# Optimization experiments

Hardware: AMD Instinct MI355X
Metric: run time of the kernel (lower is better)

The kernel has to match this reference:

```python
import jax, jax.numpy as jnp
import numpy as np

NUM_HEADS = 8
HEAD_SIZE = 64  # hidden_dim // num_heads = 512 // 8
SCALE = 1.0 / np.sqrt(HEAD_SIZE).astype(np.float32)
CAUSAL = True


def setup_inputs() -> dict:
    key = jax.random.key(0)
    k1, k2, k3 = jax.random.split(key, 3)
    b, s, d = 4, 2048, 512
    x = jax.random.normal(k1, (b, s, d), dtype=jnp.float32)
    w_qkv = jax.random.normal(k2, (d, 3 * d), dtype=jnp.float32) * 0.02
    b_qkv = jnp.zeros((3 * d,), dtype=jnp.float32)
    w_out = jax.random.normal(k3, (d, d), dtype=jnp.float32) * 0.02
    b_out = jnp.zeros((d,), dtype=jnp.float32)
    return {"x": x, "w_qkv": w_qkv, "b_qkv": b_qkv, "w_out": w_out, "b_out": b_out}


def reference(x, w_qkv, b_qkv, w_out, b_out):
    b, s, d = x.shape
    h, hd = NUM_HEADS, HEAD_SIZE
    qkv = x @ w_qkv + b_qkv                      # (b, s, 3d)
    q, k, v = jnp.split(qkv, 3, axis=-1)
    # (b, s, d) -> (b, h, s, hd)
    q = q.reshape(b, s, h, hd).transpose(0, 2, 1, 3)
    k = k.reshape(b, s, h, hd).transpose(0, 2, 1, 3)
    v = v.reshape(b, s, h, hd).transpose(0, 2, 1, 3)
    scores = jnp.einsum('bhqd,bhkd->bhqk', q, k) * SCALE  # (b, h, s, s)
    if CAUSAL:
        causal_mask = jnp.triu(jnp.ones((s, s), dtype=bool), k=1)
        scores = jnp.where(causal_mask, -jnp.inf, scores)
    attn = jax.nn.softmax(scores, axis=-1)
    out = jnp.einsum('bhqk,bhkd->bhqd', attn, v)          # (b, h, s, hd)
    out = out.transpose(0, 2, 1, 3).reshape(b, s, d)
    return out @ w_out + b_out
```

## Files before the change

### kernel.cpp

```cpp
#include <hip/hip_runtime.h>
#include <hip/hip_bf16.h>

#define BATCH 4
#define SEQ   2048
#define DM    512
#define NH    8
#define HD    64
#define PART  (BATCH*NH*SEQ*HD)
#define QSCALE 0.18033688f

typedef unsigned short u16;
typedef unsigned int   u32;
typedef __bf16 bf16x8 __attribute__((ext_vector_type(8)));
typedef float  f32x4  __attribute__((ext_vector_type(4)));
typedef float  f32x16 __attribute__((ext_vector_type(16)));
typedef unsigned int u32x2 __attribute__((ext_vector_type(2)));

__device__ __forceinline__ u16 f2bf(float f) {
    union { float f; u32 u; } v; v.f = f;
    u32 r = v.u + 0x7fffu + ((v.u >> 16) & 1u);
    return (u16)(r >> 16);
}

__device__ __forceinline__ void glds16(const u16* g, u16* lds) {
    __builtin_amdgcn_global_load_lds(
        (const __attribute__((address_space(1))) void*)g,
        (__attribute__((address_space(3))) void*)lds, 16, 0, 0);
}

__device__ __forceinline__ void pl32swap(u32 &a, u32 &b) {
    u32x2 r = __builtin_amdgcn_permlane32_swap(a, b, false, false);
    a = r[0]; b = r[1];
}

__global__ __launch_bounds__(256) void prep_k(
    const float* __restrict__ x, u16* __restrict__ xb,
    const float* __restrict__ w_qkv, u16* __restrict__ t_qkv,
    const float* __restrict__ w_out, u16* __restrict__ t_out)
{
    __shared__ u16 Ts[64][72];
    const int z = blockIdx.z, bx = blockIdx.x, t = threadIdx.x;

    if (z == 0) {
        const int n8 = PART / 8;
        for (int i = bx * 256 + t; i < n8; i += 512 * 256) {
            float4 a = *(const float4*)(x + (size_t)i * 8);
            float4 b = *(const float4*)(x + (size_t)i * 8 + 4);
            union { uint4 v; u16 s[8]; } o;
            o.s[0] = f2bf(a.x); o.s[1] = f2bf(a.y);
            o.s[2] = f2bf(a.z); o.s[3] = f2bf(a.w);
            o.s[4] = f2bf(b.x); o.s[5] = f2bf(b.y);
            o.s[6] = f2bf(b.z); o.s[7] = f2bf(b.w);
            *(uint4*)(xb + (size_t)i * 8) = o.v;
        }
        return;
    }
    const int N = (z == 1) ? 3 * DM : DM;
    const int ntiles = N / 64;
    if (bx >= ntiles * 8) return;
    const float* W = (z == 1) ? w_qkv : w_out;
    u16* Wt = (z == 1) ? t_qkv : t_out;
    const int n0 = (bx % ntiles) * 64, k0 = (bx / ntiles) * 64;

    #pragma unroll
    for (int l = 0; l < 4; ++l) {
        int idx = l * 1024 + t * 4;
        int r = idx >> 6, c = idx & 63;
        float4 v = *(const float4*)(W + (size_t)(k0 + r) * N + n0 + c);
        Ts[c + 0][r] = f2bf(v.x);
        Ts[c + 1][r] = f2bf(v.y);
        Ts[c + 2][r] = f2bf(v.z);
        Ts[c + 3][r] = f2bf(v.w);
    }
    __syncthreads();
    #pragma unroll
    for (int l = 0; l < 2; ++l) {
        int idx = l * 256 + t;
        int row = idx >> 3, ch = idx & 7;
        *(uint4*)(Wt + (size_t)(n0 + row) * DM + k0 + ch * 8) =
            *(const uint4*)(&Ts[row][ch * 8]);
    }
}

template<int MODE>
__global__ __launch_bounds__(256) void gemm_k(
    const u16* __restrict__ A, const u16* __restrict__ Bt,
    const float* __restrict__ bias, void* __restrict__ outv,
    int M, int N, int K)
{
    constexpr int BM = (MODE == 1) ? 64 : 128;
    constexpr int NI = (MODE == 1) ? 2 : 4;

    __shared__ __align__(16) u16 As[2][BM * 32];
    __shared__ __align__(16) u16 Bs[2][128 * 32];

    const int tid  = threadIdx.x;
    const int bm0  = blockIdx.x * BM;
    const int bn0  = blockIdx.y * 128;
    const int wave = tid >> 6, lane = tid & 63;
    const int l16  = lane & 15, quad = lane >> 4;
    const int wr   = (MODE == 1) ? 0 : (wave & 1) * 64;
    const int wc   = (MODE == 1) ? wave * 32 : (wave >> 1) * 64;

    const int srow = (lane >> 2);
    const int scol = (lane & 3) * 8;
    const int arow = (MODE == 1) ? (wave * 16) : (wave * 32);
    const u16* Ag = A + (size_t)(bm0 + arow + srow) * K + scol;
    const u16* Bg = Bt + (size_t)(bn0 + wave * 32 + srow) * K + scol;
    const int wofsA = arow * 32;
    const int wofsB = (wave * 32) * 32;

    f32x4 acc[4][NI];
    #pragma unroll
    for (int i = 0; i < 4; ++i)
        #pragma unroll
        for (int j = 0; j < NI; ++j)
            acc[i][j] = (f32x4){0.f, 0.f, 0.f, 0.f};

    glds16(Ag, &As[0][wofsA]);
    if (MODE == 0) glds16(Ag + (size_t)16 * K, &As[0][wofsA + 16 * 32]);
    glds16(Bg,                  &Bs[0][wofsB]);
    glds16(Bg + (size_t)16 * K, &Bs[0][wofsB + 16 * 32]);
    __syncthreads();

    const int NIT = K >> 5;
    for (int it = 0; it < NIT; ++it) {
        const int cur = it & 1;
        if (it + 1 < NIT) {
            const int nx = cur ^ 1;
            const int k0 = (it + 1) << 5;
            glds16(Ag + k0, &As[nx][wofsA]);
            if (MODE == 0) glds16(Ag + k0 + (size_t)16 * K, &As[nx][wofsA + 16 * 32]);
            glds16(Bg + k0,                  &Bs[nx][wofsB]);
            glds16(Bg + k0 + (size_t)16 * K, &Bs[nx][wofsB + 16 * 32]);
        }

        bf16x8 af[4], bfr[NI];
        #pragma unroll
        for (int mi = 0; mi < 4; ++mi)
            af[mi] = *(const bf16x8*)(&As[cur][(wr + mi * 16 + l16) * 32 + quad * 8]);
        #pragma unroll
        for (int ni = 0; ni < NI; ++ni)
            bfr[ni] = *(const bf16x8*)(&Bs[cur][(wc + ni * 16 + l16) * 32 + quad * 8]);
        #pragma unroll
        for (int mi = 0; mi < 4; ++mi)
            #pragma unroll
            for (int ni = 0; ni < NI; ++ni)
                acc[mi][ni] = __builtin_amdgcn_mfma_f32_16x16x32_bf16(
                    af[mi], bfr[ni], acc[mi][ni], 0, 0, 0);
        __syncthreads();
    }

    #pragma unroll
    for (int mi = 0; mi < 4; ++mi) {
        #pragma unroll
        for (int ni = 0; ni < NI; ++ni) {
            int col = bn0 + wc + ni * 16 + l16;
            float bv = bias[col];
            int row0 = bm0 + wr + mi * 16 + quad * 4;
            float v[4];
            #pragma unroll
            for (int reg = 0; reg < 4; ++reg) v[reg] = acc[mi][ni][reg] + bv;

            if (MODE == 1) {
                #pragma unroll
                for (int reg = 0; reg < 4; ++reg)
                    ((float*)outv)[(size_t)(row0 + reg) * N + col] = v[reg];
            } else {
                u16* ws = (u16*)outv;
                int part = col >> 9, wi = col & 511;
                int h = wi >> 6, e = wi & 63;
                int b = row0 >> 11, s0 = row0 & 2047;
                if (part == 2) {
                    union { u16 q[4]; uint2 u; } pk;
                    #pragma unroll
                    for (int reg = 0; reg < 4; ++reg) pk.q[reg] = f2bf(v[reg]);
                    *(uint2*)(ws + (size_t)2 * PART +
                              ((size_t)(b * NH + h) * HD + e) * SEQ + s0) = pk.u;
                } else {
                    float scl = (part == 0) ? QSCALE : 1.0f;
                    #pragma unroll
                    for (int reg = 0; reg < 4; ++reg)
                        ws[(size_t)part * PART +
                           ((size_t)(b * NH + h) * SEQ + s0 + reg) * HD + e] =
                            f2bf(v[reg] * scl);
                }
            }
        }
    }
}

__global__ __launch_bounds__(256, 2) void attn_k(
    const u16* __restrict__ Q, const u16* __restrict__ K,
    const u16* __restrict__ Vt, u16* __restrict__ O)
{
    __shared__ __align__(16) u16 KsB[2][64 * 64];
    __shared__ __align__(16) u16 VtB[2][64 * 64];
    __shared__ float Lred[4][32];

    const int bh   = blockIdx.x;
    const int pair = blockIdx.y;
    const int tid = threadIdx.x, wave = tid >> 6, lane = tid & 63;
    const int l31 = lane & 31, hi = lane >> 5, x7 = lane & 7;
    const int qh = wave >> 1, kh = wave & 1;
    const size_t baseK = (size_t)bh * SEQ * HD;
    const size_t baseV = (size_t)bh * HD * SEQ;
    const int b = bh >> 3, h = bh & 7;

    const int sub = lane >> 3;
    const int lcx = (lane & 7) ^ sub;
    const u16* kg = K  + baseK + (size_t)((wave * 16 + sub) * 64)   + lcx * 8;
    const u16* vg = Vt + baseV + (size_t)((wave * 16 + sub) * 2048) + lcx * 8;
    u16* ksd = &KsB[0][wave * 1024];
    u16* vtd = &VtB[0][wave * 1024];

    int koff[4], voff[2][2];
    #pragma unroll
    for (int k = 0; k < 4; ++k)
        koff[k] = (kh * 32 + l31) * 64 + ((((k << 1) + hi)) ^ x7) * 8;
    #pragma unroll
    for (int dt = 0; dt < 2; ++dt)
        #pragma unroll
        for (int k0 = 0; k0 < 2; ++k0)
            voff[dt][k0] = (dt * 32 + l31) * 64 + ((kh * 4 + k0 * 2 + hi) ^ x7) * 8;

    #pragma unroll
    for (int phase = 0; phase < 2; ++phase) {
        const int qt = phase ? pair : (31 - pair);

        const u16* qg = Q + baseK + (size_t)(qt * 64 + qh * 32 + l31) * 64 + hi * 8;
        bf16x8 qf[4];
        #pragma unroll
        for (int k = 0; k < 4; ++k)
            qf[k] = *(const bf16x8*)(qg + k * 16);

        __syncthreads();

        glds16(kg,            ksd);
        glds16(kg + 8 * 64,   ksd + 512);
        glds16(vg,            vtd);
        glds16(vg + 8 * 2048, vtd + 512);
        __syncthreads();

        float la0 = 0.f, la1 = 0.f;
        f32x16 o0, o1;
        #pragma unroll
        for (int i = 0; i < 16; ++i) { o0[i] = 0.f; o1[i] = 0.f; }

        for (int kt = 0; kt <= qt; ++kt) {
            const int cur = kt & 1;
            if (kt < qt) {
                const int nx = (cur ^ 1) * 4096;
                glds16(kg + (size_t)(kt + 1) * 4096,          ksd + nx);
                glds16(kg + (size_t)(kt + 1) * 4096 + 8 * 64, ksd + nx + 512);
                glds16(vg + (size_t)(kt + 1) * 64,            vtd + nx);
                glds16(vg + (size_t)(kt + 1) * 64 + 8 * 2048, vtd + nx + 512);
            }

            const bool diag = (kt == qt);
            if (!(diag && kh > qh)) {
                bf16x8 kf[4], vf[2][2];
                #pragma unroll
                for (int k = 0; k < 4; ++k)
                    kf[k] = *(const bf16x8*)(&KsB[cur][koff[k]]);
                #pragma unroll
                for (int dt = 0; dt < 2; ++dt)
                    #pragma unroll
                    for (int k0 = 0; k0 < 2; ++k0)
                        vf[dt][k0] = *(const bf16x8*)(&VtB[cur][voff[dt][k0]]);

                f32x16 st;
                #pragma unroll
                for (int i = 0; i < 16; ++i) st[i] = 0.f;
                #pragma unroll
                for (int k = 0; k < 4; ++k)
                    st = __builtin_amdgcn_mfma_f32_32x32x16_bf16(
                        kf[k], qf[k], st, 0, 0, 0);

                float p[16];
                #pragma unroll
                for (int r = 0; r < 16; ++r)
                    p[r] = __builtin_amdgcn_exp2f(st[r]);
                if (diag && kh == qh) {
                    #pragma unroll
                    for (int r = 0; r < 16; ++r) {
                        int kvl = (r & 3) + 8 * (r >> 2) + 4 * hi;
                        if (kvl > l31) p[r] = 0.f;
                    }
                }
                #pragma unroll
                for (int r = 0; r < 8; ++r) { la0 += p[r]; la1 += p[r + 8]; }

                u32 c[8];
                #pragma unroll
                for (int m = 0; m < 8; ++m) {
                    __hip_bfloat162 t =
                        __float22bfloat162_rn(float2{p[2 * m], p[2 * m + 1]});
                    c[m] = *(u32*)&t;
                }
                pl32swap(c[0], c[2]); pl32swap(c[1], c[3]);
                pl32swap(c[4], c[6]); pl32swap(c[5], c[7]);
                union { u32 w[4]; bf16x8 v; } pa0, pa1;
                pa0.w[0] = c[0]; pa0.w[1] = c[1]; pa0.w[2] = c[2]; pa0.w[3] = c[3];
                pa1.w[0] = c[4]; pa1.w[1] = c[5]; pa1.w[2] = c[6]; pa1.w[3] = c[7];

                o0 = __builtin_amdgcn_mfma_f32_32x32x16_bf16(pa0.v, vf[0][0], o0, 0, 0, 0);
                o0 = __builtin_amdgcn_mfma_f32_32x32x16_bf16(pa1.v, vf[0][1], o0, 0, 0, 0);
                o1 = __builtin_amdgcn_mfma_f32_32x32x16_bf16(pa0.v, vf[1][0], o1, 0, 0, 0);
                o1 = __builtin_amdgcn_mfma_f32_32x32x16_bf16(pa1.v, vf[1][1], o1, 0, 0, 0);
            }
            __syncthreads();
        }

        float l2 = (la0 + la1);
        l2 += __shfl_xor(l2, 32);
        if (lane < 32) Lred[wave][lane] = l2;
        float* Ob = (qh == 0) ? (float*)&KsB[0][0] : (float*)&VtB[0][0];
        if (kh == 1) {
            #pragma unroll
            for (int r = 0; r < 16; ++r) {
                Ob[r * 64 + lane]        = o0[r];
                Ob[(16 + r) * 64 + lane] = o1[r];
            }
        }
        __syncthreads();
        if (kh == 0) {
            #pragma unroll
            for (int r = 0; r < 16; ++r) {
                int ql = (r & 3) + 8 * (r >> 2) + 4 * hi;
                float lt = Lred[2 * qh][ql] + Lred[2 * qh + 1][ql];
                int srow = qt * 64 + qh * 32 + ql;
                size_t idx = (((size_t)(b * SEQ + srow)) * NH + h) * HD + l31;
                float v0 = (o0[r] + Ob[r * 64 + lane]) / lt;
                float v1 = (o1[r] + Ob[(16 + r) * 64 + lane]) / lt;
                O[idx]      = f2bf(v0);
                O[idx + 32] = f2bf(v1);
            }
        }
    }
}

extern "C" void kernel_launch(void* const* d_in, const int* in_sizes, int n_in,
                              void* d_out, int out_size, void* d_ws, size_t ws_size,
                              hipStream_t stream) {
    const float* x     = (const float*)d_in[0];
    const float* w_qkv = (const float*)d_in[1];
    const float* b_qkv = (const float*)d_in[2];
    const float* w_out = (const float*)d_in[3];
    const float* b_out = (const float*)d_in[4];

    u16* qkv    = (u16*)d_ws;
    u16* attn   = qkv + (size_t)3 * PART;
    u16* xb     = attn + (size_t)PART;
    u16* wt_qkv = xb + (size_t)PART;
    u16* wt_out = wt_qkv + (size_t)(3 * DM) * DM;

    const int M = BATCH * SEQ;

    prep_k<<<dim3(512, 1, 3), 256, 0, stream>>>(x, xb, w_qkv, wt_qkv,
                                                w_out, wt_out);

    dim3 g1(M / 128, (3 * DM) / 128);
    gemm_k<0><<<g1, 256, 0, stream>>>(xb, wt_qkv, b_qkv, qkv, M, 3 * DM, DM);

    dim3 g2(BATCH * NH, 16);
    attn_k<<<g2, 256, 0, stream>>>(qkv, qkv + PART, qkv + 2 * (size_t)PART, attn);

    dim3 g3(M / 64, DM / 128);
    gemm_k<1><<<g3, 256, 0, stream>>>(attn, wt_out, b_out, (float*)d_out, M, DM, DM);
}
```

Measured before the change: 146.5 us.

## Triple-buffer K/V tiles with explicit vmcnt waits and one barrier per iteration

Result: slower. 149.4 us (+2.0%).

```diff
diff --git a/kernel.cpp b/kernel.cpp
--- a/kernel.cpp
+++ b/kernel.cpp
@@ -194,8 +194,8 @@
     const u16* __restrict__ Q, const u16* __restrict__ K,
     const u16* __restrict__ Vt, u16* __restrict__ O)
 {
-    __shared__ __align__(16) u16 KsB[2][64 * 64];
-    __shared__ __align__(16) u16 VtB[2][64 * 64];
+    __shared__ __align__(16) u16 KsB[3][64 * 64];
+    __shared__ __align__(16) u16 VtB[3][64 * 64];
     __shared__ float Lred[4][32];
 
     const int bh   = blockIdx.x;
@@ -211,8 +211,8 @@
     const int lcx = (lane & 7) ^ sub;
     const u16* kg = K  + baseK + (size_t)((wave * 16 + sub) * 64)   + lcx * 8;
     const u16* vg = Vt + baseV + (size_t)((wave * 16 + sub) * 2048) + lcx * 8;
-    u16* ksd = &KsB[0][wave * 1024];
-    u16* vtd = &VtB[0][wave * 1024];
+    u16* ks0 = &KsB[0][wave * 1024];
+    u16* vt0 = &VtB[0][wave * 1024];
 
     int koff[4], voff[2][2];
     #pragma unroll
@@ -236,46 +236,64 @@
 
         __syncthreads();
 
-        glds16(kg,            ksd);
-        glds16(kg + 8 * 64,   ksd + 512);
-        glds16(vg,            vtd);
-        glds16(vg + 8 * 2048, vtd + 512);
-        __syncthreads();
+        glds16(kg,            ks0);
+        glds16(kg + 8 * 64,   ks0 + 512);
+        glds16(vg,            vt0);
+        glds16(vg + 8 * 2048, vt0 + 512);
+        if (qt >= 1) {
+            glds16(kg + 4096,          ks0 + 4096);
+            glds16(kg + 4096 + 8 * 64, ks0 + 4096 + 512);
+            glds16(vg + 64,            vt0 + 4096);
+            glds16(vg + 64 + 8 * 2048, vt0 + 4096 + 512);
+        }
 
         float la0 = 0.f, la1 = 0.f;
         f32x16 o0, o1;
         #pragma unroll
         for (int i = 0; i < 16; ++i) { o0[i] = 0.f; o1[i] = 0.f; }
 
+        int bcur = 0;
         for (int kt = 0; kt <= qt; ++kt) {
-            const int cur = kt & 1;
-            if (kt < qt) {
-                const int nx = (cur ^ 1) * 4096;
-                glds16(kg + (size_t)(kt + 1) * 4096,          ksd + nx);
-                glds16(kg + (size_t)(kt + 1) * 4096 + 8 * 64, ksd + nx + 512);
-                glds16(vg + (size_t)(kt + 1) * 64,            vtd + nx);
-                glds16(vg + (size_t)(kt + 1) * 64 + 8 * 2048, vtd + nx + 512);
+            if (kt < qt) asm volatile("s_waitcnt vmcnt(4)" ::: "memory");
+            else         asm volatile("s_waitcnt vmcnt(0)" ::: "memory");
+            __builtin_amdgcn_s_barrier();
+            asm volatile("" ::: "memory");
+
+            if (kt + 2 <= qt) {
+                int bi = bcur + 2; if (bi >= 3) bi -= 3;
+                u16* kd = ks0 + bi * 4096;
+                u16* vd = vt0 + bi * 4096;
+                const size_t ko = (size_t)(kt + 2) * 4096;
+                const size_t vo = (size_t)(kt + 2) * 64;
+                glds16(kg + ko,            kd);
+                glds16(kg + ko + 8 * 64,   kd + 512);
+                glds16(vg + vo,            vd);
+                glds16(vg + vo + 8 * 2048, vd + 512);
             }
 
             const bool diag = (kt == qt);
             if (!(diag && kh > qh)) {
+                const u16* Kb = &KsB[bcur][0];
+                const u16* Vb = &VtB[bcur][0];
                 bf16x8 kf[4], vf[2][2];
                 #pragma unroll
                 for (int k = 0; k < 4; ++k)
-                    kf[k] = *(const bf16x8*)(&KsB[cur][koff[k]]);
+                    kf[k] = *(const bf16x8*)(&Kb[koff[k]]);
                 #pragma unroll
                 for (int dt = 0; dt < 2; ++dt)
                     #pragma unroll
                     for (int k0 = 0; k0 < 2; ++k0)
-                        vf[dt][k0] = *(const bf16x8*)(&VtB[cur][voff[dt][k0]]);
+                        vf[dt][k0] = *(const bf16x8*)(&Vb[voff[dt][k0]]);
 
                 f32x16 st;
                 #pragma unroll
                 for (int i = 0; i < 16; ++i) st[i] = 0.f;
+                __builtin_amdgcn_s_setprio(1);
                 #pragma unroll
                 for (int k = 0; k < 4; ++k)
                     st = __builtin_amdgcn_mfma_f32_32x32x16_bf16(
                         kf[k], qf[k], st, 0, 0, 0);
+                __builtin_amdgcn_s_setprio(0);
 
                 float p[16];
                 #pragma unroll
@@ -304,13 +322,16 @@
                 pa0.w[0] = c[0]; pa0.w[1] = c[1]; pa0.w[2] = c[2]; pa0.w[3] = c[3];
                 pa1.w[0] = c[4]; pa1.w[1] = c[5]; pa1.w[2] = c[6]; pa1.w[3] = c[7];
 
+                __builtin_amdgcn_s_setprio(1);
                 o0 = __builtin_amdgcn_mfma_f32_32x32x16_bf16(pa0.v, vf[0][0], o0, 0, 0, 0);
                 o0 = __builtin_amdgcn_mfma_f32_32x32x16_bf16(pa1.v, vf[0][1], o0, 0, 0, 0);
                 o1 = __builtin_amdgcn_mfma_f32_32x32x16_bf16(pa0.v, vf[1][0], o1, 0, 0, 0);
                 o1 = __builtin_amdgcn_mfma_f32_32x32x16_bf16(pa1.v, vf[1][1], o1, 0, 0, 0);
-            }
-            __syncthreads();
-        }
+                __builtin_amdgcn_s_setprio(0);
+            }
+            bcur = (bcur == 2) ? 0 : bcur + 1;
+        }
+        __syncthreads();
 
         float l2 = (la0 + la1);
         l2 += __shfl_xor(l2, 32);
```
